# Kernel optimization log

Measured on AMD Instinct MI355X. Metric: run time of the kernel, lower is better.

Reference implementation:

```python
import jax, jax.numpy as jnp
import numpy as np

B, L, D, H = 4, 2048, 1024, 16
DH = D // H

def setup_inputs() -> dict:
    key = jax.random.key(0)
    k1, k2, k3 = jax.random.split(key, 3)
    x = jax.random.normal(k1, (B, L, D), dtype=jnp.float32)
    w_qkv = jax.random.normal(k2, (3 * D, D), dtype=jnp.float32) * (1.0 / np.sqrt(D))
    w_proj = jax.random.normal(k3, (D, D), dtype=jnp.float32) * (1.0 / np.sqrt(D))
    return {"x": x, "w_qkv": w_qkv, "w_proj": w_proj}

def reference(x, w_qkv, w_proj):
    b, l, d = x.shape
    scale = 1.0 / np.sqrt(DH)
    qkv = (x @ w_qkv.T).reshape(b, l, 3, H, DH)
    qkv = jnp.transpose(qkv, (2, 0, 3, 1, 4))
    q, k, v = qkv[0], qkv[1], qkv[2]
    scores = jnp.einsum('bhqd,bhkd->bhqk', q, k) * scale
    attn = jax.nn.softmax(scores, axis=-1)
    out = jnp.einsum('bhqk,bhkd->bhqd', attn, v)
    out = jnp.transpose(out, (0, 2, 1, 3)).reshape(b, l, d)
    return out @ w_proj.T
```

## Files before the change

kernel.cpp:

```cpp
#include <hip/hip_runtime.h>
#include <hip/hip_bf16.h>


typedef __bf16  bf16x8  __attribute__((ext_vector_type(8)));
typedef __bf16  bf16x4  __attribute__((ext_vector_type(4)));
typedef float   floatx4 __attribute__((ext_vector_type(4)));

__device__ __forceinline__ void async_ld16(const void* g, void* lds_base_uniform) {
  __builtin_amdgcn_global_load_lds(
      (const __attribute__((address_space(1))) void*)g,
      (__attribute__((address_space(3))) void*)lds_base_uniform,
      16, 0, 0);
}

__device__ __forceinline__ int detect_bf16(const void* p) {
  const unsigned short* u = (const unsigned short*)p;
  int sane = 0;
#pragma unroll 4
  for (int i = 0; i < 64; ++i) {
    unsigned short w = u[2 * i];
    int e = (w >> 7) & 0xFF;
    sane += (w == 0 || (e >= 100 && e <= 150)) ? 1 : 0;
  }
  return sane >= 32;
}

__device__ __forceinline__ bf16x8 ld8_f32cvt(const void* base, size_t elem) {
  const float* p = (const float*)base + elem;
  floatx4 u0 = *(const floatx4*)p;
  floatx4 u1 = *(const floatx4*)(p + 4);
  bf16x8 v;
  v[0] = (__bf16)u0[0]; v[1] = (__bf16)u0[1]; v[2] = (__bf16)u0[2]; v[3] = (__bf16)u0[3];
  v[4] = (__bf16)u1[0]; v[5] = (__bf16)u1[1]; v[6] = (__bf16)u1[2]; v[7] = (__bf16)u1[3];
  return v;
}

template<int CTRL>
__device__ __forceinline__ float dpp_f(float x) {
  return __builtin_bit_cast(float,
      __builtin_amdgcn_update_dpp(0, __builtin_bit_cast(int, x), CTRL, 0xF, 0xF, true));
}
__device__ __forceinline__ float row16_sum(float x) {
  x += dpp_f<0xB1>(x);
  x += dpp_f<0x4E>(x);
  x += dpp_f<0x141>(x);
  x += dpp_f<0x140>(x);
  return x;
}

__launch_bounds__(256)
__global__ void cvt3_kernel(const void* __restrict__ s0, __bf16* __restrict__ d0, int n0,
                            const void* __restrict__ s1, __bf16* __restrict__ d1, int n1,
                            const void* __restrict__ s2, __bf16* __restrict__ d2) {
  int u = blockIdx.x * blockDim.x + threadIdx.x;
  const void* src; __bf16* dst;
  if (u < n0)           { src = s0; dst = d0; }
  else if (u < n0 + n1) { src = s1; dst = d1; u -= n0; }
  else                  { src = s2; dst = d2; u -= n0 + n1; }
  const int is_bf16 = detect_bf16(src);
  const size_t e = (size_t)u * 8;
  if (is_bf16) *(bf16x8*)(dst + e) = *(const bf16x8*)((const __bf16*)src + e);
  else         *(bf16x8*)(dst + e) = ld8_f32cvt(src, e);
}

template<int EPI>
__launch_bounds__(256, 2)
__global__ void gemm_ptile_kernel(const __bf16* __restrict__ A,
                                  const __bf16* __restrict__ B,
                                  const void* __restrict__ oprobe,
                                  void* __restrict__ Cout,
                                  __bf16* __restrict__ qb,
                                  __bf16* __restrict__ kb,
                                  __bf16* __restrict__ vtb,
                                  int ntiles, int N)
{
  __shared__ __align__(16) __bf16 SM[4 * 8192];

  const int bx   = blockIdx.x;
  const int tid  = threadIdx.x;
  const int wave = tid >> 6;
  const int lane = tid & 63;
  const int quad = lane >> 4;
  const int l16  = lane & 15;
  const int wm   = wave >> 1;
  const int wn   = wave & 1;

  const int tb = ntiles >> 9;
  const int S  = tb << 5;

  const int srow = tid >> 2;
  const int scc  = (((tid & 3) ^ ((tid >> 3) & 3)) << 3);

  auto DECODE_M = [&](int t) { return (((t & 7) << 3) | ((t >> 3) & 7)) << 7; };
  auto DECODE_N = [&](int t) { return (t >> 6) << 7; };

  auto STAGE = [&](int s) {
    const int t  = bx + ((s >> 5) << 9);
    const int m0 = DECODE_M(t);
    const int n0 = DECODE_N(t);
    const int k0 = (s & 31) << 5;
    char* base = (char*)SM + (s & 3) * 16384;
#pragma unroll
    for (int i = 0; i < 2; ++i) {
      async_ld16(A + (size_t)(m0 + i * 64 + srow) * 1024 + k0 + scc,
                 base + i * 4096 + wave * 1024);
      async_ld16(B + (size_t)(n0 + i * 64 + srow) * 1024 + k0 + scc,
                 base + 8192 + i * 4096 + wave * 1024);
    }
  };

  const int out_bf16 = (EPI == 1) ? detect_bf16(oprobe) : 0;
  const int cswz = quad ^ ((l16 >> 1) & 3);

  floatx4 acc[4][4];
#pragma unroll
  for (int i = 0; i < 4; ++i)
#pragma unroll
    for (int j = 0; j < 4; ++j) acc[i][j] = (floatx4){0.f, 0.f, 0.f, 0.f};

  STAGE(0);
  STAGE(1);

  for (int s = 0; s < S; ++s) {
    if (s < S - 1) asm volatile("s_waitcnt vmcnt(4)" ::: "memory");
    else           asm volatile("s_waitcnt vmcnt(0)" ::: "memory");
    __builtin_amdgcn_s_barrier();
    asm volatile("" ::: "memory");

    if (s + 2 < S) STAGE(s + 2);

    const __bf16* As_ = SM + (s & 3) * 8192;
    const __bf16* Bs_ = As_ + 4096;

    bf16x8 af[4], bfr[4];
#pragma unroll
    for (int tt = 0; tt < 4; ++tt) {
      af[tt]  = *(const bf16x8*)&As_[(wm * 64 + tt * 16 + l16) * 32 + cswz * 8];
      bfr[tt] = *(const bf16x8*)&Bs_[(wn * 64 + tt * 16 + l16) * 32 + cswz * 8];
    }
    __builtin_amdgcn_s_setprio(1);
#pragma unroll
    for (int mt = 0; mt < 4; ++mt)
#pragma unroll
      for (int nt = 0; nt < 4; ++nt)
        acc[mt][nt] = __builtin_amdgcn_mfma_f32_16x16x32_bf16(af[mt], bfr[nt], acc[mt][nt], 0, 0, 0);
    __builtin_amdgcn_s_setprio(0);

    if ((s & 31) == 31) {
      const int t  = bx + ((s >> 5) << 9);
      const int m0 = DECODE_M(t);
      const int n0 = DECODE_N(t);
#pragma unroll
      for (int mt = 0; mt < 4; ++mt) {
#pragma unroll
        for (int nt = 0; nt < 4; ++nt) {
          const int n_idx = n0 + wn * 64 + nt * 16 + l16;
          const int mbase = m0 + wm * 64 + mt * 16 + quad * 4;
          if (EPI == 1) {
            if (out_bf16) {
#pragma unroll
              for (int r = 0; r < 4; ++r)
                ((__bf16*)Cout)[(size_t)(mbase + r) * N + n_idx] = (__bf16)acc[mt][nt][r];
            } else {
#pragma unroll
              for (int r = 0; r < 4; ++r)
                ((float*)Cout)[(size_t)(mbase + r) * N + n_idx] = acc[mt][nt][r];
            }
          } else {
            const int sel = n_idx >> 10;
            const int rem = n_idx & 1023;
            const int h   = rem >> 6;
            const int dh  = rem & 63;
            const int b   = mbase >> 11;
            const int l   = mbase & 2047;
            const int bh  = b * 16 + h;
            if (sel == 2) {
              bf16x4 pk;
#pragma unroll
              for (int r = 0; r < 4; ++r) pk[r] = (__bf16)acc[mt][nt][r];
              *(bf16x4*)&vtb[((size_t)bh * 64 + dh) * 2048 + l] = pk;
            } else {
              __bf16* dstb = (sel == 0 ? qb : kb) + ((size_t)bh * 2048 + l) * 64 + dh;
#pragma unroll
              for (int r = 0; r < 4; ++r)
                dstb[(size_t)r * 64] = (__bf16)acc[mt][nt][r];
            }
          }
          acc[mt][nt] = (floatx4){0.f, 0.f, 0.f, 0.f};
        }
      }
    }
  }
}

__launch_bounds__(256, 4)
__global__ void attn_kernel(const __bf16* __restrict__ qb,
                            const __bf16* __restrict__ kb,
                            const __bf16* __restrict__ vtb,
                            __bf16* __restrict__ ob )
{
  __shared__ __align__(16) __bf16 S[2][2 * 64 * 72];

  const int tid  = threadIdx.x;
  const int wave = tid >> 6;
  const int lane = tid & 63;
  const int quad = lane >> 4;
  const int l16  = lane & 15;

  const int bh = blockIdx.y;
  const int b  = bh >> 4;
  const int h  = bh & 15;
  const int q0 = blockIdx.x * 128;

  const __bf16* Qp = qb  + (size_t)bh * 2048 * 64;
  const __bf16* Kp = kb  + (size_t)bh * 2048 * 64;
  const __bf16* Vp = vtb + (size_t)bh * 64 * 2048;

  const float C1 = 0.125f * 1.44269504f;
  const float C2 = -8.0f  * 1.44269504f;

  bf16x8 aq[2][2];
#pragma unroll
  for (int rt = 0; rt < 2; ++rt) {
    const __bf16* qrow = Qp + (size_t)(q0 + wave * 32 + rt * 16 + l16) * 64;
    aq[rt][0] = *(const bf16x8*)(qrow + quad * 8);
    aq[rt][1] = *(const bf16x8*)(qrow + 32 + quad * 8);
  }

  bf16x8 onesb;
  {
    const __bf16 ov = (l16 == 0) ? (__bf16)1.0f : (__bf16)0.0f;
#pragma unroll
    for (int i = 0; i < 8; ++i) onesb[i] = ov;
  }

  floatx4 o[2][4], o5[2];
#pragma unroll
  for (int rt = 0; rt < 2; ++rt) {
    o5[rt] = (floatx4){0.f, 0.f, 0.f, 0.f};
#pragma unroll
    for (int dt = 0; dt < 4; ++dt) o[rt][dt] = (floatx4){0.f, 0.f, 0.f, 0.f};
  }

  const int sarr = wave >> 1;
  const int srb  = (wave & 1) * 32;
  const int sr0  = lane >> 3;
  const int scol = (lane & 7) * 8;

  {
    __bf16* dst = &S[0][sarr * (64 * 72)];
    if (sarr == 0) {
#pragma unroll
      for (int i = 0; i < 4; ++i) {
        const int row = srb + sr0 + 8 * i;
        *(bf16x8*)&dst[row * 72 + scol] = *(const bf16x8*)(Kp + (size_t)row * 64 + scol);
      }
    } else {
#pragma unroll
      for (int i = 0; i < 4; ++i) {
        const int row = srb + sr0 + 8 * i;
        *(bf16x8*)&dst[row * 72 + scol] = *(const bf16x8*)(Vp + (size_t)row * 2048 + scol);
      }
    }
  }
  __syncthreads();

  for (int kt = 0; kt < 32; ++kt) {
    const int cur = kt & 1;
    const int nxt = cur ^ 1;
    const int kn  = (((kt + 1) & 31) << 6);

    bf16x8 sreg[4];
    if (sarr == 0) {
#pragma unroll
      for (int i = 0; i < 4; ++i) {
        const int row = srb + sr0 + 8 * i;
        sreg[i] = *(const bf16x8*)(Kp + (size_t)(kn + row) * 64 + scol);
      }
    } else {
#pragma unroll
      for (int i = 0; i < 4; ++i) {
        const int row = srb + sr0 + 8 * i;
        sreg[i] = *(const bf16x8*)(Vp + (size_t)row * 2048 + kn + scol);
      }
    }

    const __bf16* Kc = &S[cur][0];
    const __bf16* Vc = &S[cur][64 * 72];
    __bf16*       Pq = &S[nxt][0] + wave * 2304;

    floatx4 st[2][4];
    __builtin_amdgcn_s_setprio(1);
#pragma unroll
    for (int nt = 0; nt < 4; ++nt) {
      const int krow = nt * 16 + l16;
      bf16x8 ak0 = *(const bf16x8*)&Kc[krow * 72 + quad * 8];
      bf16x8 ak1 = *(const bf16x8*)&Kc[krow * 72 + 32 + quad * 8];
#pragma unroll
      for (int rt = 0; rt < 2; ++rt) {
        floatx4 z = (floatx4){0.f, 0.f, 0.f, 0.f};
        z = __builtin_amdgcn_mfma_f32_16x16x32_bf16(ak0, aq[rt][0], z, 0, 0, 0);
        z = __builtin_amdgcn_mfma_f32_16x16x32_bf16(ak1, aq[rt][1], z, 0, 0, 0);
        st[rt][nt] = z;
      }
    }
    __builtin_amdgcn_s_setprio(0);

#pragma unroll
    for (int rt = 0; rt < 2; ++rt) {
#pragma unroll
      for (int nt = 0; nt < 4; ++nt) {
        bf16x4 pk;
#pragma unroll
        for (int r = 0; r < 4; ++r)
          pk[r] = (__bf16)__builtin_amdgcn_exp2f(fmaf(st[rt][nt][r], C1, C2));
        *(bf16x4*)&Pq[(rt * 16 + l16) * 72 + nt * 16 + quad * 4] = pk;
      }
    }

    __builtin_amdgcn_wave_barrier();

    bf16x8 ap[2][2];
#pragma unroll
    for (int rt = 0; rt < 2; ++rt) {
      ap[rt][0] = *(const bf16x8*)&Pq[(rt * 16 + l16) * 72 + quad * 8];
      ap[rt][1] = *(const bf16x8*)&Pq[(rt * 16 + l16) * 72 + 32 + quad * 8];
    }

    __builtin_amdgcn_s_setprio(1);
#pragma unroll
    for (int dt = 0; dt < 4; ++dt) {
      const int vrow = dt * 16 + l16;
      bf16x8 bv0 = *(const bf16x8*)&Vc[vrow * 72 + quad * 8];
      bf16x8 bv1 = *(const bf16x8*)&Vc[vrow * 72 + 32 + quad * 8];
#pragma unroll
      for (int rt = 0; rt < 2; ++rt) {
        o[rt][dt] = __builtin_amdgcn_mfma_f32_16x16x32_bf16(ap[rt][0], bv0, o[rt][dt], 0, 0, 0);
        o[rt][dt] = __builtin_amdgcn_mfma_f32_16x16x32_bf16(ap[rt][1], bv1, o[rt][dt], 0, 0, 0);
      }
    }
#pragma unroll
    for (int rt = 0; rt < 2; ++rt) {
      o5[rt] = __builtin_amdgcn_mfma_f32_16x16x32_bf16(ap[rt][0], onesb, o5[rt], 0, 0, 0);
      o5[rt] = __builtin_amdgcn_mfma_f32_16x16x32_bf16(ap[rt][1], onesb, o5[rt], 0, 0, 0);
    }
    __builtin_amdgcn_s_setprio(0);

    __builtin_amdgcn_wave_barrier();

    {
      __bf16* dst = &S[nxt][sarr * (64 * 72)];
#pragma unroll
      for (int i = 0; i < 4; ++i) {
        const int row = srb + sr0 + 8 * i;
        *(bf16x8*)&dst[row * 72 + scol] = sreg[i];
      }
    }
    __syncthreads();
  }

#pragma unroll
  for (int rt = 0; rt < 2; ++rt)
#pragma unroll
    for (int r = 0; r < 4; ++r) {
      const float lv  = row16_sum(l16 == 0 ? o5[rt][r] : 0.f);
      const float inv = 1.f / lv;
      const size_t rowbase =
          ((size_t)b * 2048 + q0 + wave * 32 + rt * 16 + quad * 4 + r) * 1024 + h * 64;
#pragma unroll
      for (int dt = 0; dt < 4; ++dt)
        ob[rowbase + dt * 16 + l16] = (__bf16)(o[rt][dt][r] * inv);
    }
}

extern "C" void kernel_launch(void* const* d_in, const int* in_sizes, int n_in,
                              void* d_out, int out_size, void* d_ws, size_t ws_size,
                              hipStream_t stream)
{
  (void)in_sizes; (void)n_in; (void)out_size; (void)ws_size;

  const void* x     = d_in[0];
  const void* wqkv  = d_in[1];
  const void* wproj = d_in[2];

  const size_t NX    = (size_t)8192 * 1024;
  const size_t NWQKV = (size_t)3072 * 1024;
  const size_t NWPRJ = (size_t)1024 * 1024;

  __bf16* qbuf   = (__bf16*)d_ws;
  __bf16* kbuf   = qbuf + NX;
  __bf16* vtbuf  = kbuf + NX;
  __bf16* abuf   = vtbuf + NX;
  __bf16* xb     = abuf + NX;
  __bf16* wqkvb  = xb + NX;
  __bf16* wprojb = wqkvb + NWQKV;

  dim3 blk(256);

  cvt3_kernel<<<dim3((NX + NWQKV + NWPRJ) / 2048), blk, 0, stream>>>(
      x, xb, NX / 8, wqkv, wqkvb, NWQKV / 8, wproj, wprojb);

  gemm_ptile_kernel<0><<<dim3(512), blk, 0, stream>>>(
      xb, wqkvb, nullptr, nullptr, qbuf, kbuf, vtbuf, 1536, 3072);

  attn_kernel<<<dim3(2048 / 128, 64), blk, 0, stream>>>(qbuf, kbuf, vtbuf, abuf);

  gemm_ptile_kernel<1><<<dim3(512), blk, 0, stream>>>(
      abuf, wprojb, wproj, d_out, nullptr, nullptr, nullptr, 512, 1024);
}
```

Baseline: 284.8 us.

## Fuse conversion into QKV GEMM with grid barrier, ballot-based dtype detection

Merges the fp32-to-bf16 conversion kernel into the QKV projection GEMM kernel, using a software grid-wide barrier (an atomic counter reset by a memset) between the conversion phase and the GEMM phase. This removes one kernel launch and its tail. The dtype-detection probe now reads one value per lane and combines them with a wave ballot instead of running a 64-iteration serial loop per thread. The projection GEMM is specialized with fixed sizes and a single output epilogue. The grid barrier depends on all 512 blocks being co-resident, which the occupancy of 2 per CU must guarantee, and it adds a memset launch.

New measurement: 356.3 us. +25.1%, slower.

```diff
diff --git a/kernel.cpp b/kernel.cpp
--- a/kernel.cpp
+++ b/kernel.cpp
@@ -13,16 +13,13 @@
       16, 0, 0);
 }
 
-__device__ __forceinline__ int detect_bf16(const void* p) {
+__device__ __forceinline__ int detect_bf16_wave(const void* p) {
   const unsigned short* u = (const unsigned short*)p;
-  int sane = 0;
-#pragma unroll 4
-  for (int i = 0; i < 64; ++i) {
-    unsigned short w = u[2 * i];
-    int e = (w >> 7) & 0xFF;
-    sane += (w == 0 || (e >= 100 && e <= 150)) ? 1 : 0;
-  }
-  return sane >= 32;
+  const int lane = threadIdx.x & 63;
+  const unsigned short w = u[2 * lane];
+  const int e = (w >> 7) & 0xFF;
+  const int sane = (w == 0 || (e >= 100 && e <= 150)) ? 1 : 0;
+  return __popcll(__ballot(sane)) >= 32;
 }
 
 __device__ __forceinline__ bf16x8 ld8_f32cvt(const void* base, size_t elem) {
@@ -48,31 +45,158 @@
   return x;
 }
 
-__launch_bounds__(256)
-__global__ void cvt3_kernel(const void* __restrict__ s0, __bf16* __restrict__ d0, int n0,
-                            const void* __restrict__ s1, __bf16* __restrict__ d1, int n1,
-                            const void* __restrict__ s2, __bf16* __restrict__ d2) {
-  int u = blockIdx.x * blockDim.x + threadIdx.x;
-  const void* src; __bf16* dst;
-  if (u < n0)           { src = s0; dst = d0; }
-  else if (u < n0 + n1) { src = s1; dst = d1; u -= n0; }
-  else                  { src = s2; dst = d2; u -= n0 + n1; }
-  const int is_bf16 = detect_bf16(src);
-  const size_t e = (size_t)u * 8;
-  if (is_bf16) *(bf16x8*)(dst + e) = *(const bf16x8*)((const __bf16*)src + e);
-  else         *(bf16x8*)(dst + e) = ld8_f32cvt(src, e);
-}
-
-template<int EPI>
+__device__ __forceinline__ void grid_barrier(unsigned int* ctr, unsigned int nblk) {
+  __threadfence();
+  __syncthreads();
+  if (threadIdx.x == 0) {
+    __hip_atomic_fetch_add(ctr, 1u, __ATOMIC_ACQ_REL, __HIP_MEMORY_SCOPE_AGENT);
+    while (__hip_atomic_load(ctr, __ATOMIC_ACQUIRE, __HIP_MEMORY_SCOPE_AGENT) < nblk)
+      __builtin_amdgcn_s_sleep(8);
+  }
+  __syncthreads();
+}
+
 __launch_bounds__(256, 2)
-__global__ void gemm_ptile_kernel(const __bf16* __restrict__ A,
-                                  const __bf16* __restrict__ B,
-                                  const void* __restrict__ oprobe,
-                                  void* __restrict__ Cout,
-                                  __bf16* __restrict__ qb,
-                                  __bf16* __restrict__ kb,
-                                  __bf16* __restrict__ vtb,
-                                  int ntiles, int N)
+__global__ void fused_cvt_qkv_kernel(const void* __restrict__ x,
+                                     const void* __restrict__ wqkv,
+                                     const void* __restrict__ wproj,
+                                     __bf16* __restrict__ xb,
+                                     __bf16* __restrict__ wqkvb,
+                                     __bf16* __restrict__ wprojb,
+                                     __bf16* __restrict__ qb,
+                                     __bf16* __restrict__ kb,
+                                     __bf16* __restrict__ vtb,
+                                     unsigned int* __restrict__ ctr)
+{
+  __shared__ __align__(16) __bf16 SM[4 * 8192];
+
+  const int tid = threadIdx.x;
+  const int bx  = blockIdx.x;
+
+  {
+    const int u0 = bx * 256 + tid;
+    for (int it = 0; it < 12; ++it) {
+      int u = u0 + it * (512 * 256);
+      const void* src; __bf16* dst;
+      if (u < 1048576)      { src = x;     dst = xb; }
+      else if (u < 1441792) { src = wqkv;  dst = wqkvb;  u -= 1048576; }
+      else                  { src = wproj; dst = wprojb; u -= 1441792; }
+      const int is_bf16 = detect_bf16_wave(src);
+      const size_t e = (size_t)u * 8;
+      if (is_bf16) *(bf16x8*)(dst + e) = *(const bf16x8*)((const __bf16*)src + e);
+      else         *(bf16x8*)(dst + e) = ld8_f32cvt(src, e);
+    }
+  }
+
+  grid_barrier(ctr, 512);
+
+  const int wave = tid >> 6;
+  const int lane = tid & 63;
+  const int quad = lane >> 4;
+  const int l16  = lane & 15;
+  const int wm   = wave >> 1;
+  const int wn   = wave & 1;
+
+  const int srow = tid >> 2;
+  const int scc  = (((tid & 3) ^ ((tid >> 3) & 3)) << 3);
+
+  auto DECODE_M = [&](int t) { return (((t & 7) << 3) | ((t >> 3) & 7)) << 7; };
+  auto DECODE_N = [&](int t) { return (t >> 6) << 7; };
+
+  const __bf16* A = xb;
+  const __bf16* B = wqkvb;
+
+  auto STAGE = [&](int s) {
+    const int t  = bx + ((s >> 5) << 9);
+    const int m0 = DECODE_M(t);
+    const int n0 = DECODE_N(t);
+    const int k0 = (s & 31) << 5;
+    char* base = (char*)SM + (s & 3) * 16384;
+#pragma unroll
+    for (int i = 0; i < 2; ++i) {
+      async_ld16(A + (size_t)(m0 + i * 64 + srow) * 1024 + k0 + scc,
+                 base + i * 4096 + wave * 1024);
+      async_ld16(B + (size_t)(n0 + i * 64 + srow) * 1024 + k0 + scc,
+                 base + 8192 + i * 4096 + wave * 1024);
+    }
+  };
+
+  const int cswz = quad ^ ((l16 >> 1) & 3);
+
+  floatx4 acc[4][4];
+#pragma unroll
+  for (int i = 0; i < 4; ++i)
+#pragma unroll
+    for (int j = 0; j < 4; ++j) acc[i][j] = (floatx4){0.f, 0.f, 0.f, 0.f};
+
+  STAGE(0);
+  STAGE(1);
+
+  for (int s = 0; s < 96; ++s) {
+    if (s < 95) asm volatile("s_waitcnt vmcnt(4)" ::: "memory");
+    else        asm volatile("s_waitcnt vmcnt(0)" ::: "memory");
+    __builtin_amdgcn_s_barrier();
+    asm volatile("" ::: "memory");
+
+    if (s + 2 < 96) STAGE(s + 2);
+
+    const __bf16* As_ = SM + (s & 3) * 8192;
+    const __bf16* Bs_ = As_ + 4096;
+
+    bf16x8 af[4], bfr[4];
+#pragma unroll
+    for (int tt = 0; tt < 4; ++tt) {
+      af[tt]  = *(const bf16x8*)&As_[(wm * 64 + tt * 16 + l16) * 32 + cswz * 8];
+      bfr[tt] = *(const bf16x8*)&Bs_[(wn * 64 + tt * 16 + l16) * 32 + cswz * 8];
+    }
+    __builtin_amdgcn_s_setprio(1);
+#pragma unroll
+    for (int mt = 0; mt < 4; ++mt)
+#pragma unroll
+      for (int nt = 0; nt < 4; ++nt)
+        acc[mt][nt] = __builtin_amdgcn_mfma_f32_16x16x32_bf16(af[mt], bfr[nt], acc[mt][nt], 0, 0, 0);
+    __builtin_amdgcn_s_setprio(0);
+
+    if ((s & 31) == 31) {
+      const int t  = bx + ((s >> 5) << 9);
+      const int m0 = DECODE_M(t);
+      const int n0 = DECODE_N(t);
+#pragma unroll
+      for (int mt = 0; mt < 4; ++mt) {
+#pragma unroll
+        for (int nt = 0; nt < 4; ++nt) {
+          const int n_idx = n0 + wn * 64 + nt * 16 + l16;
+          const int mbase = m0 + wm * 64 + mt * 16 + quad * 4;
+          const int sel = n_idx >> 10;
+          const int rem = n_idx & 1023;
+          const int h   = rem >> 6;
+          const int dh  = rem & 63;
+          const int b   = mbase >> 11;
+          const int l   = mbase & 2047;
+          const int bh  = b * 16 + h;
+          if (sel == 2) {
+            bf16x4 pk;
+#pragma unroll
+            for (int r = 0; r < 4; ++r) pk[r] = (__bf16)acc[mt][nt][r];
+            *(bf16x4*)&vtb[((size_t)bh * 64 + dh) * 2048 + l] = pk;
+          } else {
+            __bf16* dstb = (sel == 0 ? qb : kb) + ((size_t)bh * 2048 + l) * 64 + dh;
+#pragma unroll
+            for (int r = 0; r < 4; ++r)
+              dstb[(size_t)r * 64] = (__bf16)acc[mt][nt][r];
+          }
+          acc[mt][nt] = (floatx4){0.f, 0.f, 0.f, 0.f};
+        }
+      }
+    }
+  }
+}
+
+__launch_bounds__(256, 2)
+__global__ void gemm_proj_kernel(const __bf16* __restrict__ A,
+                                 const __bf16* __restrict__ B,
+                                 const void* __restrict__ oprobe,
+                                 void* __restrict__ Cout)
 {
   __shared__ __align__(16) __bf16 SM[4 * 8192];
 
@@ -85,19 +209,13 @@
   const int wm   = wave >> 1;
   const int wn   = wave & 1;
 
-  const int tb = ntiles >> 9;
-  const int S  = tb << 5;
-
   const int srow = tid >> 2;
   const int scc  = (((tid & 3) ^ ((tid >> 3) & 3)) << 3);
 
-  auto DECODE_M = [&](int t) { return (((t & 7) << 3) | ((t >> 3) & 7)) << 7; };
-  auto DECODE_N = [&](int t) { return (t >> 6) << 7; };
+  const int m0 = (((bx & 7) << 3) | ((bx >> 3) & 7)) << 7;
+  const int n0 = (bx >> 6) << 7;
 
   auto STAGE = [&](int s) {
-    const int t  = bx + ((s >> 5) << 9);
-    const int m0 = DECODE_M(t);
-    const int n0 = DECODE_N(t);
     const int k0 = (s & 31) << 5;
     char* base = (char*)SM + (s & 3) * 16384;
 #pragma unroll
@@ -109,7 +227,6 @@
     }
   };
 
-  const int out_bf16 = (EPI == 1) ? detect_bf16(oprobe) : 0;
   const int cswz = quad ^ ((l16 >> 1) & 3);
 
   floatx4 acc[4][4];
@@ -121,13 +238,13 @@
   STAGE(0);
   STAGE(1);
 
-  for (int s = 0; s < S; ++s) {
-    if (s < S - 1) asm volatile("s_waitcnt vmcnt(4)" ::: "memory");
-    else           asm volatile("s_waitcnt vmcnt(0)" ::: "memory");
+  for (int s = 0; s < 32; ++s) {
+    if (s < 31) asm volatile("s_waitcnt vmcnt(4)" ::: "memory");
+    else        asm volatile("s_waitcnt vmcnt(0)" ::: "memory");
     __builtin_amdgcn_s_barrier();
     asm volatile("" ::: "memory");
 
-    if (s + 2 < S) STAGE(s + 2);
+    if (s + 2 < 32) STAGE(s + 2);
 
     const __bf16* As_ = SM + (s & 3) * 8192;
     const __bf16* Bs_ = As_ + 4096;
@@ -145,49 +262,23 @@
       for (int nt = 0; nt < 4; ++nt)
         acc[mt][nt] = __builtin_amdgcn_mfma_f32_16x16x32_bf16(af[mt], bfr[nt], acc[mt][nt], 0, 0, 0);
     __builtin_amdgcn_s_setprio(0);
-
-    if ((s & 31) == 31) {
-      const int t  = bx + ((s >> 5) << 9);
-      const int m0 = DECODE_M(t);
-      const int n0 = DECODE_N(t);
-#pragma unroll
-      for (int mt = 0; mt < 4; ++mt) {
-#pragma unroll
-        for (int nt = 0; nt < 4; ++nt) {
-          const int n_idx = n0 + wn * 64 + nt * 16 + l16;
-          const int mbase = m0 + wm * 64 + mt * 16 + quad * 4;
-          if (EPI == 1) {
-            if (out_bf16) {
-#pragma unroll
-              for (int r = 0; r < 4; ++r)
-                ((__bf16*)Cout)[(size_t)(mbase + r) * N + n_idx] = (__bf16)acc[mt][nt][r];
-            } else {
-#pragma unroll
-              for (int r = 0; r < 4; ++r)
-                ((float*)Cout)[(size_t)(mbase + r) * N + n_idx] = acc[mt][nt][r];
-            }
-          } else {
-            const int sel = n_idx >> 10;
-            const int rem = n_idx & 1023;
-            const int h   = rem >> 6;
-            const int dh  = rem & 63;
-            const int b   = mbase >> 11;
-            const int l   = mbase & 2047;
-            const int bh  = b * 16 + h;
-            if (sel == 2) {
-              bf16x4 pk;
-#pragma unroll
-              for (int r = 0; r < 4; ++r) pk[r] = (__bf16)acc[mt][nt][r];
-              *(bf16x4*)&vtb[((size_t)bh * 64 + dh) * 2048 + l] = pk;
-            } else {
-              __bf16* dstb = (sel == 0 ? qb : kb) + ((size_t)bh * 2048 + l) * 64 + dh;
-#pragma unroll
-              for (int r = 0; r < 4; ++r)
-                dstb[(size_t)r * 64] = (__bf16)acc[mt][nt][r];
-            }
-          }
-          acc[mt][nt] = (floatx4){0.f, 0.f, 0.f, 0.f};
-        }
+  }
+
+  const int out_bf16 = detect_bf16_wave(oprobe);
+#pragma unroll
+  for (int mt = 0; mt < 4; ++mt) {
+#pragma unroll
+    for (int nt = 0; nt < 4; ++nt) {
+      const int n_idx = n0 + wn * 64 + nt * 16 + l16;
+      const int mbase = m0 + wm * 64 + mt * 16 + quad * 4;
+      if (out_bf16) {
+#pragma unroll
+        for (int r = 0; r < 4; ++r)
+          ((__bf16*)Cout)[(size_t)(mbase + r) * 1024 + n_idx] = (__bf16)acc[mt][nt][r];
+      } else {
+#pragma unroll
+        for (int r = 0; r < 4; ++r)
+          ((float*)Cout)[(size_t)(mbase + r) * 1024 + n_idx] = acc[mt][nt][r];
       }
     }
   }
@@ -394,17 +485,16 @@
   __bf16* xb     = abuf + NX;
   __bf16* wqkvb  = xb + NX;
   __bf16* wprojb = wqkvb + NWQKV;
+  unsigned int* ctr = (unsigned int*)(wprojb + NWPRJ);
 
   dim3 blk(256);
 
-  cvt3_kernel<<<dim3((NX + NWQKV + NWPRJ) / 2048), blk, 0, stream>>>(
-      x, xb, NX / 8, wqkv, wqkvb, NWQKV / 8, wproj, wprojb);
-
-  gemm_ptile_kernel<0><<<dim3(512), blk, 0, stream>>>(
-      xb, wqkvb, nullptr, nullptr, qbuf, kbuf, vtbuf, 1536, 3072);
+  hipMemsetAsync(ctr, 0, 64, stream);
+
+  fused_cvt_qkv_kernel<<<dim3(512), blk, 0, stream>>>(
+      x, wqkv, wproj, xb, wqkvb, wprojb, qbuf, kbuf, vtbuf, ctr);
 
   attn_kernel<<<dim3(2048 / 128, 64), blk, 0, stream>>>(qbuf, kbuf, vtbuf, abuf);
 
-  gemm_ptile_kernel<1><<<dim3(512), blk, 0, stream>>>(
-      abuf, wprojb, wproj, d_out, nullptr, nullptr, nullptr, 512, 1024);
-}
+  gemm_proj_kernel<<<dim3(512), blk, 0, stream>>>(abuf, wprojb, wproj, d_out);
+}
```

## Use 256x128 eight-wave QKV GEMM with triple-buffered BK=64 pipeline

Applied to the files above, without the earlier changes.

Replaces the persistent 128x128 QKV GEMM with a dedicated 512-thread kernel. Each block computes a 256x128 tile with BK=64 using triple-buffered async LDS loads, interleaves global stages across four MFMA sub-phases, and maps blocks to XCDs. It also replaces the per-thread 64-load bf16 format probe with a single load per lane plus a wave ballot, and specialises the projection GEMM to one tile per block. The larger tile is meant to raise data reuse and cut loop overhead, but it allows only one block per CU and adds more barriers per iteration.

Result: faster. 268.0 us (-5.9%).

```diff
diff --git a/kernel.cpp b/kernel.cpp
--- a/kernel.cpp
+++ b/kernel.cpp
@@ -13,16 +13,13 @@
       16, 0, 0);
 }
 
-__device__ __forceinline__ int detect_bf16(const void* p) {
+__device__ __forceinline__ int detect_bf16_wave(const void* p) {
   const unsigned short* u = (const unsigned short*)p;
-  int sane = 0;
-#pragma unroll 4
-  for (int i = 0; i < 64; ++i) {
-    unsigned short w = u[2 * i];
-    int e = (w >> 7) & 0xFF;
-    sane += (w == 0 || (e >= 100 && e <= 150)) ? 1 : 0;
-  }
-  return sane >= 32;
+  const int lane = threadIdx.x & 63;
+  const unsigned short w = u[2 * lane];
+  const int e = (w >> 7) & 0xFF;
+  const int sane = (w == 0 || (e >= 100 && e <= 150)) ? 1 : 0;
+  return __popcll(__ballot(sane)) >= 32;
 }
 
 __device__ __forceinline__ bf16x8 ld8_f32cvt(const void* base, size_t elem) {
@@ -57,22 +54,176 @@
   if (u < n0)           { src = s0; dst = d0; }
   else if (u < n0 + n1) { src = s1; dst = d1; u -= n0; }
   else                  { src = s2; dst = d2; u -= n0 + n1; }
-  const int is_bf16 = detect_bf16(src);
+  const int is_bf16 = detect_bf16_wave(src);
   const size_t e = (size_t)u * 8;
   if (is_bf16) *(bf16x8*)(dst + e) = *(const bf16x8*)((const __bf16*)src + e);
   else         *(bf16x8*)(dst + e) = ld8_f32cvt(src, e);
 }
 
-template<int EPI>
+__launch_bounds__(512, 1)
+__global__ void gemm_qkv8_kernel(const __bf16* __restrict__ A,
+                                 const __bf16* __restrict__ B,
+                                 __bf16* __restrict__ qb,
+                                 __bf16* __restrict__ kb,
+                                 __bf16* __restrict__ vtb)
+{
+  __shared__ __align__(16) __bf16 SM[3 * 24576];
+
+  const int flat = blockIdx.x;
+  const int xcd  = flat & 7;
+  const int j    = flat >> 3;
+  const int m0   = ((xcd << 2) | (j & 3)) << 8;
+  const int n0   = (j >> 2) << 7;
+
+  const int tid  = threadIdx.x;
+  const int wave = tid >> 6;
+  const int lane = tid & 63;
+  const int quad = lane >> 4;
+  const int l16  = lane & 15;
+  const int wm   = wave >> 1;
+  const int wn   = wave & 1;
+
+  auto STAGE_A = [&](int kt2, int a) {
+    const int s   = a * 512 + tid;
+    const int row = s >> 3;
+    const int col = ((s & 7) ^ (row & 7)) << 3;
+    async_ld16(A + (size_t)(m0 + row) * 1024 + (kt2 << 6) + col,
+               (char*)SM + (kt2 % 3) * 49152 + (a * 512 + wave * 64) * 16);
+  };
+  auto STAGE_B = [&](int kt2, int b) {
+    const int s   = b * 512 + tid;
+    const int row = s >> 3;
+    const int col = ((s & 7) ^ (row & 7)) << 3;
+    async_ld16(B + (size_t)(n0 + row) * 1024 + (kt2 << 6) + col,
+               (char*)SM + (kt2 % 3) * 49152 + 32768 + (b * 512 + wave * 64) * 16);
+  };
+
+  floatx4 acc[4][4];
+#pragma unroll
+  for (int i = 0; i < 4; ++i)
+#pragma unroll
+    for (int nf = 0; nf < 4; ++nf) acc[i][nf] = (floatx4){0.f, 0.f, 0.f, 0.f};
+
+#pragma unroll
+  for (int a = 0; a < 4; ++a) STAGE_A(0, a);
+#pragma unroll
+  for (int b = 0; b < 2; ++b) STAGE_B(0, b);
+#pragma unroll
+  for (int a = 0; a < 4; ++a) STAGE_A(1, a);
+#pragma unroll
+  for (int b = 0; b < 2; ++b) STAGE_B(1, b);
+
+  for (int kt = 0; kt < 16; ++kt) {
+    const __bf16* SL = SM + (kt % 3) * 24576;
+    const int go = (kt < 14);
+
+    auto RA = [&](int mf, int ks) {
+      const int row = wm * 64 + mf * 16 + l16;
+      return *(const bf16x8*)&SL[row * 64 + (((ks << 2) | quad) ^ (row & 7)) * 8];
+    };
+    auto RB = [&](int nf, int ks) {
+      const int row = wn * 64 + nf * 16 + l16;
+      return *(const bf16x8*)&SL[16384 + row * 64 + (((ks << 2) | quad) ^ (row & 7)) * 8];
+    };
+
+    if (kt < 15) asm volatile("s_waitcnt vmcnt(6)" ::: "memory");
+    else         asm volatile("s_waitcnt vmcnt(0)" ::: "memory");
+    __builtin_amdgcn_s_barrier();
+    asm volatile("" ::: "memory");
+
+    bf16x8 a0[4];
+#pragma unroll
+    for (int mf = 0; mf < 4; ++mf) a0[mf] = RA(mf, 0);
+    bf16x8 b00 = RB(0, 0), b10 = RB(1, 0);
+    if (go) { STAGE_A(kt + 2, 0); STAGE_A(kt + 2, 1); }
+    asm volatile("s_waitcnt lgkmcnt(0)" ::: "memory");
+    __builtin_amdgcn_sched_barrier(0);
+    __builtin_amdgcn_s_setprio(1);
+#pragma unroll
+    for (int mf = 0; mf < 4; ++mf) {
+      acc[mf][0] = __builtin_amdgcn_mfma_f32_16x16x32_bf16(a0[mf], b00, acc[mf][0], 0, 0, 0);
+      acc[mf][1] = __builtin_amdgcn_mfma_f32_16x16x32_bf16(a0[mf], b10, acc[mf][1], 0, 0, 0);
+    }
+    __builtin_amdgcn_s_setprio(0);
+    __builtin_amdgcn_s_barrier();
+    asm volatile("" ::: "memory");
+
+    bf16x8 b20 = RB(2, 0), b30 = RB(3, 0);
+    if (go) { STAGE_A(kt + 2, 2); STAGE_A(kt + 2, 3); }
+    asm volatile("s_waitcnt lgkmcnt(0)" ::: "memory");
+    __builtin_amdgcn_sched_barrier(0);
+    __builtin_amdgcn_s_setprio(1);
+#pragma unroll
+    for (int mf = 0; mf < 4; ++mf) {
+      acc[mf][2] = __builtin_amdgcn_mfma_f32_16x16x32_bf16(a0[mf], b20, acc[mf][2], 0, 0, 0);
+      acc[mf][3] = __builtin_amdgcn_mfma_f32_16x16x32_bf16(a0[mf], b30, acc[mf][3], 0, 0, 0);
+    }
+    __builtin_amdgcn_s_setprio(0);
+    __builtin_amdgcn_s_barrier();
+    asm volatile("" ::: "memory");
+
+    bf16x8 a1[4];
+#pragma unroll
+    for (int mf = 0; mf < 4; ++mf) a1[mf] = RA(mf, 1);
+    bf16x8 b01 = RB(0, 1), b11 = RB(1, 1);
+    if (go) { STAGE_B(kt + 2, 0); STAGE_B(kt + 2, 1); }
+    asm volatile("s_waitcnt lgkmcnt(0)" ::: "memory");
+    __builtin_amdgcn_sched_barrier(0);
+    __builtin_amdgcn_s_setprio(1);
+#pragma unroll
+    for (int mf = 0; mf < 4; ++mf) {
+      acc[mf][0] = __builtin_amdgcn_mfma_f32_16x16x32_bf16(a1[mf], b01, acc[mf][0], 0, 0, 0);
+      acc[mf][1] = __builtin_amdgcn_mfma_f32_16x16x32_bf16(a1[mf], b11, acc[mf][1], 0, 0, 0);
+    }
+    __builtin_amdgcn_s_setprio(0);
+    __builtin_amdgcn_s_barrier();
+    asm volatile("" ::: "memory");
+
+    bf16x8 b21 = RB(2, 1), b31 = RB(3, 1);
+    asm volatile("s_waitcnt lgkmcnt(0)" ::: "memory");
+    __builtin_amdgcn_sched_barrier(0);
+    __builtin_amdgcn_s_setprio(1);
+#pragma unroll
+    for (int mf = 0; mf < 4; ++mf) {
+      acc[mf][2] = __builtin_amdgcn_mfma_f32_16x16x32_bf16(a1[mf], b21, acc[mf][2], 0, 0, 0);
+      acc[mf][3] = __builtin_amdgcn_mfma_f32_16x16x32_bf16(a1[mf], b31, acc[mf][3], 0, 0, 0);
+    }
+    __builtin_amdgcn_s_setprio(0);
+  }
+
+#pragma unroll
+  for (int mf = 0; mf < 4; ++mf) {
+#pragma unroll
+    for (int nf = 0; nf < 4; ++nf) {
+      const int n_idx = n0 + wn * 64 + nf * 16 + l16;
+      const int mbase = m0 + wm * 64 + mf * 16 + quad * 4;
+      const int sel = n_idx >> 10;
+      const int rem = n_idx & 1023;
+      const int h   = rem >> 6;
+      const int dh  = rem & 63;
+      const int b   = mbase >> 11;
+      const int l   = mbase & 2047;
+      const int bh  = b * 16 + h;
+      if (sel == 2) {
+        bf16x4 pk;
+#pragma unroll
+        for (int r = 0; r < 4; ++r) pk[r] = (__bf16)acc[mf][nf][r];
+        *(bf16x4*)&vtb[((size_t)bh * 64 + dh) * 2048 + l] = pk;
+      } else {
+        __bf16* dstb = (sel == 0 ? qb : kb) + ((size_t)bh * 2048 + l) * 64 + dh;
+#pragma unroll
+        for (int r = 0; r < 4; ++r)
+          dstb[(size_t)r * 64] = (__bf16)acc[mf][nf][r];
+      }
+    }
+  }
+}
+
 __launch_bounds__(256, 2)
-__global__ void gemm_ptile_kernel(const __bf16* __restrict__ A,
-                                  const __bf16* __restrict__ B,
-                                  const void* __restrict__ oprobe,
-                                  void* __restrict__ Cout,
-                                  __bf16* __restrict__ qb,
-                                  __bf16* __restrict__ kb,
-                                  __bf16* __restrict__ vtb,
-                                  int ntiles, int N)
+__global__ void gemm_proj_kernel(const __bf16* __restrict__ A,
+                                 const __bf16* __restrict__ B,
+                                 const void* __restrict__ oprobe,
+                                 void* __restrict__ Cout)
 {
   __shared__ __align__(16) __bf16 SM[4 * 8192];
 
@@ -85,19 +236,13 @@
   const int wm   = wave >> 1;
   const int wn   = wave & 1;
 
-  const int tb = ntiles >> 9;
-  const int S  = tb << 5;
-
   const int srow = tid >> 2;
   const int scc  = (((tid & 3) ^ ((tid >> 3) & 3)) << 3);
 
-  auto DECODE_M = [&](int t) { return (((t & 7) << 3) | ((t >> 3) & 7)) << 7; };
-  auto DECODE_N = [&](int t) { return (t >> 6) << 7; };
+  const int m0 = (((bx & 7) << 3) | ((bx >> 3) & 7)) << 7;
+  const int n0 = (bx >> 6) << 7;
 
   auto STAGE = [&](int s) {
-    const int t  = bx + ((s >> 5) << 9);
-    const int m0 = DECODE_M(t);
-    const int n0 = DECODE_N(t);
     const int k0 = (s & 31) << 5;
     char* base = (char*)SM + (s & 3) * 16384;
 #pragma unroll
@@ -109,7 +254,6 @@
     }
   };
 
-  const int out_bf16 = (EPI == 1) ? detect_bf16(oprobe) : 0;
   const int cswz = quad ^ ((l16 >> 1) & 3);
 
   floatx4 acc[4][4];
@@ -121,13 +265,13 @@
   STAGE(0);
   STAGE(1);
 
-  for (int s = 0; s < S; ++s) {
-    if (s < S - 1) asm volatile("s_waitcnt vmcnt(4)" ::: "memory");
-    else           asm volatile("s_waitcnt vmcnt(0)" ::: "memory");
+  for (int s = 0; s < 32; ++s) {
+    if (s < 31) asm volatile("s_waitcnt vmcnt(4)" ::: "memory");
+    else        asm volatile("s_waitcnt vmcnt(0)" ::: "memory");
     __builtin_amdgcn_s_barrier();
     asm volatile("" ::: "memory");
 
-    if (s + 2 < S) STAGE(s + 2);
+    if (s + 2 < 32) STAGE(s + 2);
 
     const __bf16* As_ = SM + (s & 3) * 8192;
     const __bf16* Bs_ = As_ + 4096;
@@ -145,49 +289,23 @@
       for (int nt = 0; nt < 4; ++nt)
         acc[mt][nt] = __builtin_amdgcn_mfma_f32_16x16x32_bf16(af[mt], bfr[nt], acc[mt][nt], 0, 0, 0);
     __builtin_amdgcn_s_setprio(0);
-
-    if ((s & 31) == 31) {
-      const int t  = bx + ((s >> 5) << 9);
-      const int m0 = DECODE_M(t);
-      const int n0 = DECODE_N(t);
-#pragma unroll
-      for (int mt = 0; mt < 4; ++mt) {
-#pragma unroll
-        for (int nt = 0; nt < 4; ++nt) {
-          const int n_idx = n0 + wn * 64 + nt * 16 + l16;
-          const int mbase = m0 + wm * 64 + mt * 16 + quad * 4;
-          if (EPI == 1) {
-            if (out_bf16) {
-#pragma unroll
-              for (int r = 0; r < 4; ++r)
-                ((__bf16*)Cout)[(size_t)(mbase + r) * N + n_idx] = (__bf16)acc[mt][nt][r];
-            } else {
-#pragma unroll
-              for (int r = 0; r < 4; ++r)
-                ((float*)Cout)[(size_t)(mbase + r) * N + n_idx] = acc[mt][nt][r];
-            }
-          } else {
-            const int sel = n_idx >> 10;
-            const int rem = n_idx & 1023;
-            const int h   = rem >> 6;
-            const int dh  = rem & 63;
-            const int b   = mbase >> 11;
-            const int l   = mbase & 2047;
-            const int bh  = b * 16 + h;
-            if (sel == 2) {
-              bf16x4 pk;
-#pragma unroll
-              for (int r = 0; r < 4; ++r) pk[r] = (__bf16)acc[mt][nt][r];
-              *(bf16x4*)&vtb[((size_t)bh * 64 + dh) * 2048 + l] = pk;
-            } else {
-              __bf16* dstb = (sel == 0 ? qb : kb) + ((size_t)bh * 2048 + l) * 64 + dh;
-#pragma unroll
-              for (int r = 0; r < 4; ++r)
-                dstb[(size_t)r * 64] = (__bf16)acc[mt][nt][r];
-            }
-          }
-          acc[mt][nt] = (floatx4){0.f, 0.f, 0.f, 0.f};
-        }
+  }
+
+  const int out_bf16 = detect_bf16_wave(oprobe);
+#pragma unroll
+  for (int mt = 0; mt < 4; ++mt) {
+#pragma unroll
+    for (int nt = 0; nt < 4; ++nt) {
+      const int n_idx = n0 + wn * 64 + nt * 16 + l16;
+      const int mbase = m0 + wm * 64 + mt * 16 + quad * 4;
+      if (out_bf16) {
+#pragma unroll
+        for (int r = 0; r < 4; ++r)
+          ((__bf16*)Cout)[(size_t)(mbase + r) * 1024 + n_idx] = (__bf16)acc[mt][nt][r];
+      } else {
+#pragma unroll
+        for (int r = 0; r < 4; ++r)
+          ((float*)Cout)[(size_t)(mbase + r) * 1024 + n_idx] = acc[mt][nt][r];
       }
     }
   }
@@ -395,16 +513,13 @@
   __bf16* wqkvb  = xb + NX;
   __bf16* wprojb = wqkvb + NWQKV;
 
-  dim3 blk(256);
-
-  cvt3_kernel<<<dim3((NX + NWQKV + NWPRJ) / 2048), blk, 0, stream>>>(
+  cvt3_kernel<<<dim3((NX + NWQKV + NWPRJ) / 2048), dim3(256), 0, stream>>>(
       x, xb, NX / 8, wqkv, wqkvb, NWQKV / 8, wproj, wprojb);
 
-  gemm_ptile_kernel<0><<<dim3(512), blk, 0, stream>>>(
-      xb, wqkvb, nullptr, nullptr, qbuf, kbuf, vtbuf, 1536, 3072);
-
-  attn_kernel<<<dim3(2048 / 128, 64), blk, 0, stream>>>(qbuf, kbuf, vtbuf, abuf);
-
-  gemm_ptile_kernel<1><<<dim3(512), blk, 0, stream>>>(
-      abuf, wprojb, wproj, d_out, nullptr, nullptr, nullptr, 512, 1024);
-}
+  gemm_qkv8_kernel<<<dim3(768), dim3(512), 0, stream>>>(
+      xb, wqkvb, qbuf, kbuf, vtbuf);
+
+  attn_kernel<<<dim3(2048 / 128, 64), dim3(256), 0, stream>>>(qbuf, kbuf, vtbuf, abuf);
+
+  gemm_proj_kernel<<<dim3(512), dim3(256), 0, stream>>>(abuf, wprojb, wproj, d_out);
+}
```
